# Kernel optimization log

Measured on AMD Instinct MI355X. Metric: run time of the kernel, lower is better.

Reference implementation:

```python
import jax, jax.numpy as jnp
import numpy as np
from jax import lax

B, S, NX, NSFC, H, NY = 8192, 64, 4, 5, 32, 1


def _lstm(x, h0, c0, w_ih, w_hh, b_ih, b_hh):
    """batch_first LSTM, PyTorch gate order (i, f, g, o).
    x: [B,S,I]; h0,c0: [B,H]; w_ih: [4H,I]; w_hh: [4H,H]. Returns [B,S,H]."""
    # Precompute the input projection for all timesteps (big GEMM, once).
    xg = jnp.einsum('bsi,gi->bsg', x, w_ih) + b_ih + b_hh  # [B,S,4H]

    def step(carry, xg_t):
        h, c = carry
        gates = xg_t + h @ w_hh.T  # [B,4H]
        i, f, g, o = jnp.split(gates, 4, axis=-1)
        i = jax.nn.sigmoid(i)
        f = jax.nn.sigmoid(f)
        g = jnp.tanh(g)
        o = jax.nn.sigmoid(o)
        c = f * c + i * g
        h = o * jnp.tanh(c)
        return (h, c), h

    (_, _), hs = lax.scan(step, (h0, c0), jnp.swapaxes(xg, 0, 1))  # hs: [S,B,H]
    return jnp.swapaxes(hs, 0, 1)


def setup_inputs() -> dict:
    key = jax.random.key(0)
    ks = jax.random.split(key, 16)
    s = 1.0 / np.sqrt(H)

    def u(k, shape):
        return jax.random.uniform(k, shape, jnp.float32, -s, s)

    return {
        'inputs_main': jax.random.normal(ks[0], (B, S, NX), jnp.float32),
        'inputs_sfc': jax.random.normal(ks[1], (B, NSFC), jnp.float32),
        'w_sfc1': u(ks[2], (H, NSFC)), 'b_sfc1': u(ks[3], (H,)),
        'w_sfc2': u(ks[4], (H, NSFC)), 'b_sfc2': u(ks[5], (H,)),
        'w_ih1': u(ks[6], (4 * H, NX)), 'w_hh1': u(ks[7], (4 * H, H)),
        'b_ih1': u(ks[8], (4 * H,)), 'b_hh1': u(ks[9], (4 * H,)),
        'w_ih2': u(ks[10], (4 * H, H)), 'w_hh2': u(ks[11], (4 * H, H)),
        'b_ih2': u(ks[12], (4 * H,)), 'b_hh2': u(ks[13], (4 * H,)),
        'w_out': u(ks[14], (NY, H)), 'b_out': u(ks[15], (NY,)),
    }


def reference(inputs_main, inputs_sfc,
              w_sfc1, b_sfc1, w_sfc2, b_sfc2,
              w_ih1, w_hh1, b_ih1, b_hh1,
              w_ih2, w_hh2, b_ih2, b_hh2,
              w_out, b_out):
    # Surface MLPs -> initial (h0, c0) of rnn1
    h0 = jnp.tanh(inputs_sfc @ w_sfc1.T + b_sfc1)  # [B,H]
    c0 = jnp.tanh(inputs_sfc @ w_sfc2.T + b_sfc2)  # [B,H]

    # rnn1 runs on time-reversed input; its output is flipped back
    x = jnp.flip(inputs_main, axis=1)
    out = _lstm(x, h0, c0, w_ih1, w_hh1, b_ih1, b_hh1)
    out = jnp.flip(out, axis=1)

    # rnn2 with zero initial state (PyTorch default)
    z = jnp.zeros((out.shape[0], H), out.dtype)
    out2 = _lstm(out, z, z, w_ih2, w_hh2, b_ih2, b_hh2)

    # Output MLP (concat=False -> last layer output only)
    return out2 @ w_out.T + b_out  # [B,S,NY]
```

## Files before the change

### kernel.cpp

```cpp
#include <hip/hip_runtime.h>

typedef __attribute__((ext_vector_type(4))) float f32x4;
typedef __attribute__((ext_vector_type(8))) short bf16x8;

#define LOG2E 1.44269504088896340736f

__device__ __forceinline__ float bcf(unsigned u){ union{unsigned u;float f;}v; v.u=u; return v.f; }
__device__ __forceinline__ unsigned pkbf(float a, float b){
    unsigned w; asm("v_cvt_pk_bf16_f32 %0, %1, %2" : "=v"(w) : "v"(a), "v"(b)); return w;
}
__device__ __forceinline__ float ex2(float x){ return __builtin_amdgcn_exp2f(x); }
__device__ __forceinline__ float rcp_(float x){ return __builtin_amdgcn_rcpf(x); }

#define MFMA(a,b,c) __builtin_amdgcn_mfma_f32_16x16x32_bf16(a,b,c,0,0,0)

union FragU { unsigned w[4]; bf16x8 v; };

__device__ __forceinline__ void split8(const float* v, bf16x8 &fh, bf16x8 &fl){
    FragU H, L;
#pragma unroll
    for (int i=0;i<4;i++){
        unsigned w = pkbf(v[2*i], v[2*i+1]);
        H.w[i] = w;
        float ra = v[2*i]   - bcf(w<<16);
        float rb = v[2*i+1] - bcf(w & 0xffff0000u);
        L.w[i] = pkbf(ra, rb);
    }
    fh = H.v; fl = L.v;
}

__device__ __forceinline__ void build_bx(const float4& x, int hi, FragU& B){
    unsigned w0 = pkbf(x.x, x.y), w1 = pkbf(x.z, x.w);
    float r0 = x.x - bcf(w0<<16), r1 = x.y - bcf(w0 & 0xffff0000u);
    float r2 = x.z - bcf(w1<<16), r3 = x.w - bcf(w1 & 0xffff0000u);
    unsigned l0 = pkbf(r0,r1), l1 = pkbf(r2,r3);
    const bool h01 = (hi < 2);
    B.w[0] = h01 ? w0 : 0u;
    B.w[1] = h01 ? w1 : 0u;
    B.w[2] = (hi==0) ? l0 : (hi==1 ? 0x3f803f80u : 0u);
    B.w[3] = (hi==0) ? l1 : 0u;
}

__device__ __forceinline__ void write_h(unsigned (*hb)[16][20], int b15, int hi, int wv_,
                                        const float* hv){
    unsigned h0 = pkbf(hv[0], hv[1]);
    unsigned h1 = pkbf(hv[2], hv[3]);
    float r0 = hv[0]-bcf(h0<<16), r1 = hv[1]-bcf(h0 & 0xffff0000u);
    float r2 = hv[2]-bcf(h1<<16), r3 = hv[3]-bcf(h1 & 0xffff0000u);
    unsigned l0 = pkbf(r0,r1), l1 = pkbf(r2,r3);
    const int wi = 8*wv_ + 2*hi;
    *(uint2*)&hb[0][b15][wi] = make_uint2(h0,h1);
    *(uint2*)&hb[1][b15][wi] = make_uint2(l0,l1);
}

__global__ __launch_bounds__(128) void lstm2_mfma2(
    const float* __restrict__ xin,
    const float* __restrict__ sfc,
    const float* __restrict__ w_sfc1, const float* __restrict__ b_sfc1,
    const float* __restrict__ w_sfc2, const float* __restrict__ b_sfc2,
    const float* __restrict__ w_ih1, const float* __restrict__ w_hh1,
    const float* __restrict__ b_ih1, const float* __restrict__ b_hh1,
    const float* __restrict__ w_ih2, const float* __restrict__ w_hh2,
    const float* __restrict__ b_ih2, const float* __restrict__ b_hh2,
    const float* __restrict__ w_out, const float* __restrict__ b_out,
    float* __restrict__ outp)
{
    __shared__ __align__(16) unsigned out1q[64][16][16];
    __shared__ __align__(16) unsigned hbuf[2][2][16][20];
    __shared__ float ybuf[2][64][16];

    const int tid  = threadIdx.x;
    const int wv   = tid >> 6;
    const int lane = tid & 63;
    const int b15  = lane & 15;
    const int hi   = (lane >> 4) & 3;
    const int B0   = blockIdx.x * 16;

    bf16x8 Whh_h[4], Whh_l[4], WxA[4];
    bf16x8 W2h_h[4], W2h_l[4], W2x_h[4], W2x_l[4];
    float bia[4][4], woutr[4];
#pragma unroll
    for (int c=0;c<4;c++){
        const int gr = 32*c + 16*wv + b15;
        const float sc = (c==2) ? (2.0f*LOG2E) : (-LOG2E);
        float wvv[8];
        {
            float4 wa = *(const float4*)(w_hh1 + gr*32 + 8*hi);
            float4 wb = *(const float4*)(w_hh1 + gr*32 + 8*hi + 4);
            wvv[0]=wa.x*sc; wvv[1]=wa.y*sc; wvv[2]=wa.z*sc; wvv[3]=wa.w*sc;
            wvv[4]=wb.x*sc; wvv[5]=wb.y*sc; wvv[6]=wb.z*sc; wvv[7]=wb.w*sc;
        }
        split8(wvv, Whh_h[c], Whh_l[c]);
        {
            float4 wi = *(const float4*)(w_ih1 + gr*4);
            float wh0=wi.x*sc, wh1=wi.y*sc, wh2=wi.z*sc, wh3=wi.w*sc;
            unsigned xw0 = pkbf(wh0,wh1), xw1 = pkbf(wh2,wh3);
            float wl0 = wh0-bcf(xw0<<16), wl1 = wh1-bcf(xw0 & 0xffff0000u);
            float wl2 = wh2-bcf(xw1<<16), wl3 = wh3-bcf(xw1 & 0xffff0000u);
            unsigned lw0 = pkbf(wl0,wl1), lw1 = pkbf(wl2,wl3);
            float bias = (b_ih1[gr] + b_hh1[gr])*sc;
            unsigned bh = pkbf(bias, 0.0f);
            float blo = bias - bcf(bh<<16);
            unsigned bword = pkbf(bias, blo);
            FragU A;
            if (hi==0){ A.w[0]=xw0; A.w[1]=xw1; A.w[2]=xw0; A.w[3]=xw1; }
            else if (hi==1){ A.w[0]=lw0; A.w[1]=lw1; A.w[2]=bword; A.w[3]=0u; }
            else { A.w[0]=0u; A.w[1]=0u; A.w[2]=0u; A.w[3]=0u; }
            WxA[c] = A.v;
        }
        {
            float4 wa = *(const float4*)(w_hh2 + gr*32 + 8*hi);
            float4 wb = *(const float4*)(w_hh2 + gr*32 + 8*hi + 4);
            wvv[0]=wa.x*sc; wvv[1]=wa.y*sc; wvv[2]=wa.z*sc; wvv[3]=wa.w*sc;
            wvv[4]=wb.x*sc; wvv[5]=wb.y*sc; wvv[6]=wb.z*sc; wvv[7]=wb.w*sc;
        }
        split8(wvv, W2h_h[c], W2h_l[c]);
        {
            const float scx = sc * (1.0f/32767.0f);
            float4 wa = *(const float4*)(w_ih2 + gr*32 + 8*hi);
            float4 wb = *(const float4*)(w_ih2 + gr*32 + 8*hi + 4);
            wvv[0]=wa.x*scx; wvv[1]=wa.y*scx; wvv[2]=wa.z*scx; wvv[3]=wa.w*scx;
            wvv[4]=wb.x*scx; wvv[5]=wb.y*scx; wvv[6]=wb.z*scx; wvv[7]=wb.w*scx;
        }
        split8(wvv, W2x_h[c], W2x_l[c]);
    }
#pragma unroll
    for (int p=0;p<4;p++){
        const int j = 16*wv + 4*hi + p;
        bia[0][p] = (b_ih2[j]    + b_hh2[j])    * (-LOG2E);
        bia[1][p] = (b_ih2[32+j] + b_hh2[32+j]) * (-LOG2E);
        bia[2][p] = (b_ih2[64+j] + b_hh2[64+j]) * (2.0f*LOG2E);
        bia[3][p] = (b_ih2[96+j] + b_hh2[96+j]) * (-LOG2E);
        woutr[p]  = w_out[j];
    }

    float cs[4], hv[4];
    {
        const float* sp = sfc + (B0 + b15)*5;
        const float s0=sp[0], s1=sp[1], s2=sp[2], s3=sp[3], s4=sp[4];
#pragma unroll
        for (int p=0;p<4;p++){
            const int j = 16*wv + 4*hi + p;
            float a1 = b_sfc1[j] + s0*w_sfc1[j*5+0] + s1*w_sfc1[j*5+1]
                     + s2*w_sfc1[j*5+2] + s3*w_sfc1[j*5+3] + s4*w_sfc1[j*5+4];
            float a2 = b_sfc2[j] + s0*w_sfc2[j*5+0] + s1*w_sfc2[j*5+1]
                     + s2*w_sfc2[j*5+2] + s3*w_sfc2[j*5+3] + s4*w_sfc2[j*5+4];
            hv[p] = 1.0f - 2.0f*rcp_(ex2((2.0f*LOG2E)*a1)+1.0f);
            cs[p] = (2.0f*LOG2E)*(1.0f - 2.0f*rcp_(ex2((2.0f*LOG2E)*a2)+1.0f));
        }
    }
    write_h(hbuf[0], b15, hi, wv, hv);
    __syncthreads();

    int par = 0;
    FragU Bx;
    {
        float4 x0 = *(const float4*)(xin + ((B0 + b15)*64 + 63)*4);
        build_bx(x0, hi, Bx);
    }
#pragma unroll 1
    for (int t=63; t>=0; --t){
        bf16x8 Hh = *(const bf16x8*)&hbuf[par][0][b15][4*hi];
        bf16x8 Hl = *(const bf16x8*)&hbuf[par][1][b15][4*hi];
        f32x4 acc[4];
#pragma unroll
        for (int c=0;c<4;c++){
            f32x4 a = {0.f,0.f,0.f,0.f};
            a = MFMA(WxA[c],   Bx.v, a);
            a = MFMA(Whh_h[c], Hh,   a);
            a = MFMA(Whh_h[c], Hl,   a);
            a = MFMA(Whh_l[c], Hh,   a);
            acc[c] = a;
        }
        if (t){
            float4 xn = *(const float4*)(xin + ((B0 + b15)*64 + (t-1))*4);
            build_bx(xn, hi, Bx);
        }
        int q[4];
#pragma unroll
        for (int p=0;p<4;p++){
            float iv = acc[0][p], fv = acc[1][p], gv = acc[2][p], ov = acc[3][p];
            float si = rcp_(1.0f+ex2(iv));
            float sf = rcp_(1.0f+ex2(fv));
            float so = rcp_(1.0f+ex2(ov));
            float tg = 1.0f - 2.0f*rcp_(ex2(gv)+1.0f);
            cs[p] = fmaf(sf, cs[p], ((2.0f*LOG2E)*si)*tg);
            float tc = 1.0f - 2.0f*rcp_(ex2(cs[p])+1.0f);
            hv[p] = so*tc;
            q[p] = __float2int_rn(hv[p]*32767.0f);
        }
        unsigned q01 = ((unsigned)q[0] & 0xffffu) | ((unsigned)q[1] << 16);
        unsigned q23 = ((unsigned)q[2] & 0xffffu) | ((unsigned)q[3] << 16);
        *(uint2*)&out1q[t][b15][8*wv + 2*hi] = make_uint2(q01, q23);
        write_h(hbuf[par^1], b15, hi, wv, hv);
        __syncthreads();
        par ^= 1;
    }

    {
        const int wi = 8*wv + 2*hi;
        *(uint2*)&hbuf[par][0][b15][wi] = make_uint2(0u,0u);
        *(uint2*)&hbuf[par][1][b15][wi] = make_uint2(0u,0u);
        cs[0]=0.f; cs[1]=0.f; cs[2]=0.f; cs[3]=0.f;
    }
    FragU Xh, Xl;
    {
        const uint4 xw = *(const uint4*)&out1q[0][b15][4*hi];
        float xv[8];
        xv[0]=(float)(short)(xw.x & 0xffffu); xv[1]=(float)((int)xw.x >> 16);
        xv[2]=(float)(short)(xw.y & 0xffffu); xv[3]=(float)((int)xw.y >> 16);
        xv[4]=(float)(short)(xw.z & 0xffffu); xv[5]=(float)((int)xw.z >> 16);
        xv[6]=(float)(short)(xw.w & 0xffffu); xv[7]=(float)((int)xw.w >> 16);
        split8(xv, Xh.v, Xl.v);
    }
    __syncthreads();

#pragma unroll 1
    for (int t=0; t<64; ++t){
        bf16x8 Hh = *(const bf16x8*)&hbuf[par][0][b15][4*hi];
        bf16x8 Hl = *(const bf16x8*)&hbuf[par][1][b15][4*hi];
        f32x4 acc[4];
#pragma unroll
        for (int c=0;c<4;c++){
            f32x4 a = {0.f,0.f,0.f,0.f};
            a = MFMA(W2x_h[c], Xh.v, a);
            a = MFMA(W2x_h[c], Xl.v, a);
            a = MFMA(W2x_l[c], Xh.v, a);
            a = MFMA(W2h_h[c], Hh,   a);
            a = MFMA(W2h_h[c], Hl,   a);
            a = MFMA(W2h_l[c], Hh,   a);
            acc[c] = a;
        }
        const int tn = (t < 63) ? t+1 : 63;
        const uint4 xw = *(const uint4*)&out1q[tn][b15][4*hi];

        float y = 0.0f;
#pragma unroll
        for (int p=0;p<4;p++){
            float iv = acc[0][p] + bia[0][p];
            float fv = acc[1][p] + bia[1][p];
            float gv = acc[2][p] + bia[2][p];
            float ov = acc[3][p] + bia[3][p];
            float si = rcp_(1.0f+ex2(iv));
            float sf = rcp_(1.0f+ex2(fv));
            float so = rcp_(1.0f+ex2(ov));
            float tg = 1.0f - 2.0f*rcp_(ex2(gv)+1.0f);
            cs[p] = fmaf(sf, cs[p], ((2.0f*LOG2E)*si)*tg);
            float tc = 1.0f - 2.0f*rcp_(ex2(cs[p])+1.0f);
            hv[p] = so*tc;
            y = fmaf(hv[p], woutr[p], y);
        }
        y += __shfl_xor(y, 16, 64);
        y += __shfl_xor(y, 32, 64);
        if (hi == 0) ybuf[wv][t][b15] = y;
        write_h(hbuf[par^1], b15, hi, wv, hv);
        {
            float xv[8];
            xv[0]=(float)(short)(xw.x & 0xffffu); xv[1]=(float)((int)xw.x >> 16);
            xv[2]=(float)(short)(xw.y & 0xffffu); xv[3]=(float)((int)xw.y >> 16);
            xv[4]=(float)(short)(xw.z & 0xffffu); xv[5]=(float)((int)xw.z >> 16);
            xv[6]=(float)(short)(xw.w & 0xffffu); xv[7]=(float)((int)xw.w >> 16);
            split8(xv, Xh.v, Xl.v);
        }
        __syncthreads();
        par ^= 1;
    }

    const float bo = b_out[0];
    const int bb = tid >> 3;
    const int t0 = (tid & 7) * 8;
#pragma unroll
    for (int hlf=0; hlf<2; ++hlf){
        float4 v;
        v.x = ybuf[0][t0+4*hlf+0][bb] + ybuf[1][t0+4*hlf+0][bb] + bo;
        v.y = ybuf[0][t0+4*hlf+1][bb] + ybuf[1][t0+4*hlf+1][bb] + bo;
        v.z = ybuf[0][t0+4*hlf+2][bb] + ybuf[1][t0+4*hlf+2][bb] + bo;
        v.w = ybuf[0][t0+4*hlf+3][bb] + ybuf[1][t0+4*hlf+3][bb] + bo;
        *(float4*)(outp + (B0 + bb)*64 + t0 + 4*hlf) = v;
    }
}

extern "C" void kernel_launch(void* const* d_in, const int* in_sizes, int n_in,
                              void* d_out, int out_size, void* d_ws, size_t ws_size,
                              hipStream_t stream) {
    const float* xin    = (const float*)d_in[0];
    const float* sfc    = (const float*)d_in[1];
    const float* w_sfc1 = (const float*)d_in[2];
    const float* b_sfc1 = (const float*)d_in[3];
    const float* w_sfc2 = (const float*)d_in[4];
    const float* b_sfc2 = (const float*)d_in[5];
    const float* w_ih1  = (const float*)d_in[6];
    const float* w_hh1  = (const float*)d_in[7];
    const float* b_ih1  = (const float*)d_in[8];
    const float* b_hh1  = (const float*)d_in[9];
    const float* w_ih2  = (const float*)d_in[10];
    const float* w_hh2  = (const float*)d_in[11];
    const float* b_ih2  = (const float*)d_in[12];
    const float* b_hh2  = (const float*)d_in[13];
    const float* w_out  = (const float*)d_in[14];
    const float* b_out  = (const float*)d_in[15];
    float* out = (float*)d_out;

    dim3 grid(8192 / 16);
    dim3 block(128);
    hipLaunchKernelGGL(lstm2_mfma2, grid, block, 0, stream,
                       xin, sfc, w_sfc1, b_sfc1, w_sfc2, b_sfc2,
                       w_ih1, w_hh1, b_ih1, b_hh1,
                       w_ih2, w_hh2, b_ih2, b_hh2,
                       w_out, b_out, out);
}
```

Baseline: 175.1 us.

## Split gate work across four waves and spill layer-1 output to workspace

Adds a 256-thread kernel where each of four waves computes two gate-column MFMA tiles instead of four, with the gate layout rearranged so each lane holds all four gates of one hidden unit. The quantized layer-1 hidden sequence now goes to a global workspace instead of a 64 KB shared buffer, which cuts LDS use per block so more blocks can be resident. Layer-2 weights are loaded after layer 1 to lower register pressure. The old kernel is kept as a fallback when the workspace is too small. The costs are global-memory round trips for the layer-1 sequence and scalar 16-bit LDS stores for the hidden state.

After: 182.6 us. +4.3%, slower.

```diff
diff --git a/kernel.cpp b/kernel.cpp
--- a/kernel.cpp
+++ b/kernel.cpp
@@ -41,21 +41,265 @@
     B.w[3] = (hi==0) ? l1 : 0u;
 }
 
-__device__ __forceinline__ void write_h(unsigned (*hb)[16][20], int b15, int hi, int wv_,
-                                        const float* hv){
-    unsigned h0 = pkbf(hv[0], hv[1]);
-    unsigned h1 = pkbf(hv[2], hv[3]);
-    float r0 = hv[0]-bcf(h0<<16), r1 = hv[1]-bcf(h0 & 0xffff0000u);
-    float r2 = hv[2]-bcf(h1<<16), r3 = hv[3]-bcf(h1 & 0xffff0000u);
+__device__ __forceinline__ void put_h(unsigned* Hh, unsigned* Hl, int col, int j, float h){
+    unsigned w  = pkbf(h, 0.0f);
+    float  rr   = h - bcf(w << 16);
+    unsigned lw = pkbf(rr, 0.0f);
+    ((unsigned short*)Hh)[col*40 + j] = (unsigned short)w;
+    ((unsigned short*)Hl)[col*40 + j] = (unsigned short)lw;
+}
+
+__global__ __launch_bounds__(256) void lstm2_q(
+    const float* __restrict__ xin,
+    const float* __restrict__ sfc,
+    const float* __restrict__ w_sfc1, const float* __restrict__ b_sfc1,
+    const float* __restrict__ w_sfc2, const float* __restrict__ b_sfc2,
+    const float* __restrict__ w_ih1, const float* __restrict__ w_hh1,
+    const float* __restrict__ b_ih1, const float* __restrict__ b_hh1,
+    const float* __restrict__ w_ih2, const float* __restrict__ w_hh2,
+    const float* __restrict__ b_ih2, const float* __restrict__ b_hh2,
+    const float* __restrict__ w_out, const float* __restrict__ b_out,
+    float* __restrict__ outp,
+    unsigned* __restrict__ ws)
+{
+    __shared__ __align__(16) unsigned hbuf[2][2][16][20];
+    __shared__ float ybuf[4][64][16];
+
+    const int tid  = threadIdx.x;
+    const int wq   = tid >> 6;
+    const int lane = tid & 63;
+    const int col  = lane & 15;
+    const int hi   = lane >> 4;
+    const int B0   = blockIdx.x * 16;
+    unsigned* wsb  = ws + blockIdx.x * 16384;
+
+    const int jl = col >> 2, g = col & 3;
+    const float sc = (g == 2) ? (2.0f*LOG2E) : (-LOG2E);
+    const int j0 = 8*wq + hi;
+    const int j1 = 8*wq + 4 + hi;
+
+    bf16x8 Whh_h[2], Whh_l[2], WxA[2];
+#pragma unroll
+    for (int c=0;c<2;c++){
+        const int grow = g*32 + 8*wq + 4*c + jl;
+        float wvv[8];
+        float4 wa = *(const float4*)(w_hh1 + grow*32 + 8*hi);
+        float4 wb = *(const float4*)(w_hh1 + grow*32 + 8*hi + 4);
+        wvv[0]=wa.x*sc; wvv[1]=wa.y*sc; wvv[2]=wa.z*sc; wvv[3]=wa.w*sc;
+        wvv[4]=wb.x*sc; wvv[5]=wb.y*sc; wvv[6]=wb.z*sc; wvv[7]=wb.w*sc;
+        split8(wvv, Whh_h[c], Whh_l[c]);
+        float4 wi = *(const float4*)(w_ih1 + grow*4);
+        float wh0=wi.x*sc, wh1=wi.y*sc, wh2=wi.z*sc, wh3=wi.w*sc;
+        unsigned xw0 = pkbf(wh0,wh1), xw1 = pkbf(wh2,wh3);
+        float wl0 = wh0-bcf(xw0<<16), wl1 = wh1-bcf(xw0 & 0xffff0000u);
+        float wl2 = wh2-bcf(xw1<<16), wl3 = wh3-bcf(xw1 & 0xffff0000u);
+        unsigned lw0 = pkbf(wl0,wl1), lw1 = pkbf(wl2,wl3);
+        float bias = (b_ih1[grow] + b_hh1[grow])*sc;
+        unsigned bh = pkbf(bias, 0.0f);
+        float blo = bias - bcf(bh<<16);
+        unsigned bword = pkbf(bias, blo);
+        FragU A;
+        if (hi==0){ A.w[0]=xw0; A.w[1]=xw1; A.w[2]=xw0; A.w[3]=xw1; }
+        else if (hi==1){ A.w[0]=lw0; A.w[1]=lw1; A.w[2]=bword; A.w[3]=0u; }
+        else { A.w[0]=0u; A.w[1]=0u; A.w[2]=0u; A.w[3]=0u; }
+        WxA[c] = A.v;
+    }
+
+    float cs[2], hv[2];
+    {
+        const float* sp = sfc + (B0 + col)*5;
+        const float s0=sp[0], s1=sp[1], s2=sp[2], s3=sp[3], s4=sp[4];
+#pragma unroll
+        for (int c=0;c<2;c++){
+            const int j = 8*wq + 4*c + hi;
+            float a1 = b_sfc1[j] + s0*w_sfc1[j*5+0] + s1*w_sfc1[j*5+1]
+                     + s2*w_sfc1[j*5+2] + s3*w_sfc1[j*5+3] + s4*w_sfc1[j*5+4];
+            float a2 = b_sfc2[j] + s0*w_sfc2[j*5+0] + s1*w_sfc2[j*5+1]
+                     + s2*w_sfc2[j*5+2] + s3*w_sfc2[j*5+3] + s4*w_sfc2[j*5+4];
+            hv[c] = 1.0f - 2.0f*rcp_(ex2((2.0f*LOG2E)*a1)+1.0f);
+            cs[c] = (2.0f*LOG2E)*(1.0f - 2.0f*rcp_(ex2((2.0f*LOG2E)*a2)+1.0f));
+        }
+    }
+    put_h(&hbuf[0][0][0][0], &hbuf[0][1][0][0], col, j0, hv[0]);
+    put_h(&hbuf[0][0][0][0], &hbuf[0][1][0][0], col, j1, hv[1]);
+    __syncthreads();
+
+    int par = 0;
+    FragU Bx;
+    {
+        float4 x0 = *(const float4*)(xin + ((B0 + col)*64 + 63)*4);
+        build_bx(x0, hi, Bx);
+    }
+#pragma unroll 1
+    for (int t=63; t>=0; --t){
+        bf16x8 Hh = *(const bf16x8*)&hbuf[par][0][col][4*hi];
+        bf16x8 Hl = *(const bf16x8*)&hbuf[par][1][col][4*hi];
+        f32x4 acc[2];
+#pragma unroll
+        for (int c=0;c<2;c++){
+            f32x4 a = {0.f,0.f,0.f,0.f};
+            a = MFMA(WxA[c],   Bx.v, a);
+            a = MFMA(Whh_h[c], Hh,   a);
+            a = MFMA(Whh_h[c], Hl,   a);
+            a = MFMA(Whh_l[c], Hh,   a);
+            acc[c] = a;
+        }
+        if (t){
+            float4 xn = *(const float4*)(xin + ((B0 + col)*64 + (t-1))*4);
+            build_bx(xn, hi, Bx);
+        }
+        int q[2];
+#pragma unroll
+        for (int c=0;c<2;c++){
+            float iv = acc[c][0], fv = acc[c][1], gv = acc[c][2], ov = acc[c][3];
+            float si = rcp_(1.0f+ex2(iv));
+            float sf = rcp_(1.0f+ex2(fv));
+            float so = rcp_(1.0f+ex2(ov));
+            float tg = 1.0f - 2.0f*rcp_(ex2(gv)+1.0f);
+            cs[c] = fmaf(sf, cs[c], ((2.0f*LOG2E)*si)*tg);
+            float tc = 1.0f - 2.0f*rcp_(ex2(cs[c])+1.0f);
+            hv[c] = so*tc;
+            q[c] = __float2int_rn(hv[c]*32767.0f);
+        }
+        put_h(&hbuf[par^1][0][0][0], &hbuf[par^1][1][0][0], col, j0, hv[0]);
+        put_h(&hbuf[par^1][0][0][0], &hbuf[par^1][1][0][0], col, j1, hv[1]);
+        {
+            int e0 = __shfl_xor(q[0], 16, 64);
+            int e1 = __shfl_xor(q[1], 16, 64);
+            unsigned val = (hi & 1)
+                ? (((unsigned)e1 & 0xffffu) | ((unsigned)q[1] << 16))
+                : (((unsigned)q[0] & 0xffffu) | ((unsigned)e0 << 16));
+            const int word = 4*wq + 2*(hi & 1) + (hi >> 1);
+            wsb[(t*16 + col)*16 + word] = val;
+        }
+        __syncthreads();
+        par ^= 1;
+    }
+
+    bf16x8 W2h_h[2], W2h_l[2], W2x_h[2], W2x_l[2];
+#pragma unroll
+    for (int c=0;c<2;c++){
+        const int grow = g*32 + 8*wq + 4*c + jl;
+        float wvv[8];
+        {
+            float4 wa = *(const float4*)(w_hh2 + grow*32 + 8*hi);
+            float4 wb = *(const float4*)(w_hh2 + grow*32 + 8*hi + 4);
+            wvv[0]=wa.x*sc; wvv[1]=wa.y*sc; wvv[2]=wa.z*sc; wvv[3]=wa.w*sc;
+            wvv[4]=wb.x*sc; wvv[5]=wb.y*sc; wvv[6]=wb.z*sc; wvv[7]=wb.w*sc;
+        }
+        split8(wvv, W2h_h[c], W2h_l[c]);
+        {
+            const float scx = sc * (1.0f/32767.0f);
+            float4 wa = *(const float4*)(w_ih2 + grow*32 + 8*hi);
+            float4 wb = *(const float4*)(w_ih2 + grow*32 + 8*hi + 4);
+            wvv[0]=wa.x*scx; wvv[1]=wa.y*scx; wvv[2]=wa.z*scx; wvv[3]=wa.w*scx;
+            wvv[4]=wb.x*scx; wvv[5]=wb.y*scx; wvv[6]=wb.z*scx; wvv[7]=wb.w*scx;
+        }
+        split8(wvv, W2x_h[c], W2x_l[c]);
+    }
+    float bia[2][4], woutr[2];
+#pragma unroll
+    for (int c=0;c<2;c++){
+        const int j = 8*wq + 4*c + hi;
+#pragma unroll
+        for (int p=0;p<4;p++){
+            const float s = (p==2) ? (2.0f*LOG2E) : (-LOG2E);
+            bia[c][p] = (b_ih2[p*32+j] + b_hh2[p*32+j]) * s;
+        }
+        woutr[c] = w_out[j];
+        cs[c] = 0.0f;
+    }
+    put_h(&hbuf[par][0][0][0], &hbuf[par][1][0][0], col, j0, 0.0f);
+    put_h(&hbuf[par][0][0][0], &hbuf[par][1][0][0], col, j1, 0.0f);
+    FragU Xh, Xl;
+    {
+        const uint4 xw = *(const uint4*)&wsb[(0*16 + col)*16 + 4*hi];
+        float xv[8];
+        xv[0]=(float)(short)(xw.x & 0xffffu); xv[1]=(float)((int)xw.x >> 16);
+        xv[2]=(float)(short)(xw.y & 0xffffu); xv[3]=(float)((int)xw.y >> 16);
+        xv[4]=(float)(short)(xw.z & 0xffffu); xv[5]=(float)((int)xw.z >> 16);
+        xv[6]=(float)(short)(xw.w & 0xffffu); xv[7]=(float)((int)xw.w >> 16);
+        split8(xv, Xh.v, Xl.v);
+    }
+    __syncthreads();
+
+#pragma unroll 1
+    for (int t=0; t<64; ++t){
+        bf16x8 Hh = *(const bf16x8*)&hbuf[par][0][col][4*hi];
+        bf16x8 Hl = *(const bf16x8*)&hbuf[par][1][col][4*hi];
+        f32x4 acc[2];
+#pragma unroll
+        for (int c=0;c<2;c++){
+            f32x4 a = {0.f,0.f,0.f,0.f};
+            a = MFMA(W2x_h[c], Xh.v, a);
+            a = MFMA(W2x_h[c], Xl.v, a);
+            a = MFMA(W2x_l[c], Xh.v, a);
+            a = MFMA(W2h_h[c], Hh,   a);
+            a = MFMA(W2h_h[c], Hl,   a);
+            a = MFMA(W2h_l[c], Hh,   a);
+            acc[c] = a;
+        }
+        const int tn = (t < 63) ? t+1 : 63;
+        const uint4 xw = *(const uint4*)&wsb[(tn*16 + col)*16 + 4*hi];
+
+        float y = 0.0f;
+#pragma unroll
+        for (int c=0;c<2;c++){
+            float iv = acc[c][0] + bia[c][0];
+            float fv = acc[c][1] + bia[c][1];
+            float gv = acc[c][2] + bia[c][2];
+            float ov = acc[c][3] + bia[c][3];
+            float si = rcp_(1.0f+ex2(iv));
+            float sf = rcp_(1.0f+ex2(fv));
+            float so = rcp_(1.0f+ex2(ov));
+            float tg = 1.0f - 2.0f*rcp_(ex2(gv)+1.0f);
+            cs[c] = fmaf(sf, cs[c], ((2.0f*LOG2E)*si)*tg);
+            float tc = 1.0f - 2.0f*rcp_(ex2(cs[c])+1.0f);
+            hv[c] = so*tc;
+            y = fmaf(hv[c], woutr[c], y);
+        }
+        y += __shfl_xor(y, 16, 64);
+        y += __shfl_xor(y, 32, 64);
+        if (hi == 0) ybuf[wq][t][col] = y;
+        put_h(&hbuf[par^1][0][0][0], &hbuf[par^1][1][0][0], col, j0, hv[0]);
+        put_h(&hbuf[par^1][0][0][0], &hbuf[par^1][1][0][0], col, j1, hv[1]);
+        {
+            float xv[8];
+            xv[0]=(float)(short)(xw.x & 0xffffu); xv[1]=(float)((int)xw.x >> 16);
+            xv[2]=(float)(short)(xw.y & 0xffffu); xv[3]=(float)((int)xw.y >> 16);
+            xv[4]=(float)(short)(xw.z & 0xffffu); xv[5]=(float)((int)xw.z >> 16);
+            xv[6]=(float)(short)(xw.w & 0xffffu); xv[7]=(float)((int)xw.w >> 16);
+            split8(xv, Xh.v, Xl.v);
+        }
+        __syncthreads();
+        par ^= 1;
+    }
+
+    const float bo = b_out[0];
+    const int bb = tid >> 4;
+    const int t0 = (tid & 15) * 4;
+    float4 v;
+    v.x = ybuf[0][t0+0][bb]+ybuf[1][t0+0][bb]+ybuf[2][t0+0][bb]+ybuf[3][t0+0][bb]+bo;
+    v.y = ybuf[0][t0+1][bb]+ybuf[1][t0+1][bb]+ybuf[2][t0+1][bb]+ybuf[3][t0+1][bb]+bo;
+    v.z = ybuf[0][t0+2][bb]+ybuf[1][t0+2][bb]+ybuf[2][t0+2][bb]+ybuf[3][t0+2][bb]+bo;
+    v.w = ybuf[0][t0+3][bb]+ybuf[1][t0+3][bb]+ybuf[2][t0+3][bb]+ybuf[3][t0+3][bb]+bo;
+    *(float4*)(outp + (B0 + bb)*64 + t0) = v;
+}
+
+__device__ __forceinline__ void write_h_pair(unsigned (*hb)[16][20], int b15, int hi, int wv_,
+                                             const float* hvv){
+    unsigned h0 = pkbf(hvv[0], hvv[1]);
+    unsigned h1 = pkbf(hvv[2], hvv[3]);
+    float r0 = hvv[0]-bcf(h0<<16), r1 = hvv[1]-bcf(h0 & 0xffff0000u);
+    float r2 = hvv[2]-bcf(h1<<16), r3 = hvv[3]-bcf(h1 & 0xffff0000u);
     unsigned l0 = pkbf(r0,r1), l1 = pkbf(r2,r3);
     const int wi = 8*wv_ + 2*hi;
     *(uint2*)&hb[0][b15][wi] = make_uint2(h0,h1);
     *(uint2*)&hb[1][b15][wi] = make_uint2(l0,l1);
 }
 
-__global__ __launch_bounds__(128) void lstm2_mfma2(
-    const float* __restrict__ xin,
-    const float* __restrict__ sfc,
+__global__ __launch_bounds__(128) void lstm2_fb(
+    const float* __restrict__ xin, const float* __restrict__ sfc,
     const float* __restrict__ w_sfc1, const float* __restrict__ b_sfc1,
     const float* __restrict__ w_sfc2, const float* __restrict__ b_sfc2,
     const float* __restrict__ w_ih1, const float* __restrict__ w_hh1,
@@ -68,14 +312,12 @@
     __shared__ __align__(16) unsigned out1q[64][16][16];
     __shared__ __align__(16) unsigned hbuf[2][2][16][20];
     __shared__ float ybuf[2][64][16];
-
     const int tid  = threadIdx.x;
     const int wv   = tid >> 6;
     const int lane = tid & 63;
     const int b15  = lane & 15;
     const int hi   = (lane >> 4) & 3;
     const int B0   = blockIdx.x * 16;
-
     bf16x8 Whh_h[4], Whh_l[4], WxA[4];
     bf16x8 W2h_h[4], W2h_l[4], W2x_h[4], W2x_l[4];
     float bia[4][4], woutr[4];
@@ -133,8 +375,7 @@
         bia[3][p] = (b_ih2[96+j] + b_hh2[96+j]) * (-LOG2E);
         woutr[p]  = w_out[j];
     }
-
-    float cs[4], hv[4];
+    float cs[4], hvv[4];
     {
         const float* sp = sfc + (B0 + b15)*5;
         const float s0=sp[0], s1=sp[1], s2=sp[2], s3=sp[3], s4=sp[4];
@@ -145,13 +386,12 @@
                      + s2*w_sfc1[j*5+2] + s3*w_sfc1[j*5+3] + s4*w_sfc1[j*5+4];
             float a2 = b_sfc2[j] + s0*w_sfc2[j*5+0] + s1*w_sfc2[j*5+1]
                      + s2*w_sfc2[j*5+2] + s3*w_sfc2[j*5+3] + s4*w_sfc2[j*5+4];
-            hv[p] = 1.0f - 2.0f*rcp_(ex2((2.0f*LOG2E)*a1)+1.0f);
+            hvv[p] = 1.0f - 2.0f*rcp_(ex2((2.0f*LOG2E)*a1)+1.0f);
             cs[p] = (2.0f*LOG2E)*(1.0f - 2.0f*rcp_(ex2((2.0f*LOG2E)*a2)+1.0f));
         }
     }
-    write_h(hbuf[0], b15, hi, wv, hv);
+    write_h_pair(hbuf[0], b15, hi, wv, hvv);
     __syncthreads();
-
     int par = 0;
     FragU Bx;
     {
@@ -186,17 +426,16 @@
             float tg = 1.0f - 2.0f*rcp_(ex2(gv)+1.0f);
             cs[p] = fmaf(sf, cs[p], ((2.0f*LOG2E)*si)*tg);
             float tc = 1.0f - 2.0f*rcp_(ex2(cs[p])+1.0f);
-            hv[p] = so*tc;
-            q[p] = __float2int_rn(hv[p]*32767.0f);
+            hvv[p] = so*tc;
+            q[p] = __float2int_rn(hvv[p]*32767.0f);
         }
         unsigned q01 = ((unsigned)q[0] & 0xffffu) | ((unsigned)q[1] << 16);
         unsigned q23 = ((unsigned)q[2] & 0xffffu) | ((unsigned)q[3] << 16);
         *(uint2*)&out1q[t][b15][8*wv + 2*hi] = make_uint2(q01, q23);
-        write_h(hbuf[par^1], b15, hi, wv, hv);
+        write_h_pair(hbuf[par^1], b15, hi, wv, hvv);
         __syncthreads();
         par ^= 1;
     }
-
     {
         const int wi = 8*wv + 2*hi;
         *(uint2*)&hbuf[par][0][b15][wi] = make_uint2(0u,0u);
@@ -214,7 +453,6 @@
         split8(xv, Xh.v, Xl.v);
     }
     __syncthreads();
-
 #pragma unroll 1
     for (int t=0; t<64; ++t){
         bf16x8 Hh = *(const bf16x8*)&hbuf[par][0][b15][4*hi];
@@ -233,7 +471,6 @@
         }
         const int tn = (t < 63) ? t+1 : 63;
         const uint4 xw = *(const uint4*)&out1q[tn][b15][4*hi];
-
         float y = 0.0f;
 #pragma unroll
         for (int p=0;p<4;p++){
@@ -247,13 +484,13 @@
             float tg = 1.0f - 2.0f*rcp_(ex2(gv)+1.0f);
             cs[p] = fmaf(sf, cs[p], ((2.0f*LOG2E)*si)*tg);
             float tc = 1.0f - 2.0f*rcp_(ex2(cs[p])+1.0f);
-            hv[p] = so*tc;
-            y = fmaf(hv[p], woutr[p], y);
+            hvv[p] = so*tc;
+            y = fmaf(hvv[p], woutr[p], y);
         }
         y += __shfl_xor(y, 16, 64);
         y += __shfl_xor(y, 32, 64);
         if (hi == 0) ybuf[wv][t][b15] = y;
-        write_h(hbuf[par^1], b15, hi, wv, hv);
+        write_h_pair(hbuf[par^1], b15, hi, wv, hvv);
         {
             float xv[8];
             xv[0]=(float)(short)(xw.x & 0xffffu); xv[1]=(float)((int)xw.x >> 16);
@@ -265,7 +502,6 @@
         __syncthreads();
         par ^= 1;
     }
-
     const float bo = b_out[0];
     const int bb = tid >> 3;
     const int t0 = (tid & 7) * 8;
@@ -301,11 +537,18 @@
     const float* b_out  = (const float*)d_in[15];
     float* out = (float*)d_out;
 
-    dim3 grid(8192 / 16);
-    dim3 block(128);
-    hipLaunchKernelGGL(lstm2_mfma2, grid, block, 0, stream,
-                       xin, sfc, w_sfc1, b_sfc1, w_sfc2, b_sfc2,
-                       w_ih1, w_hh1, b_ih1, b_hh1,
-                       w_ih2, w_hh2, b_ih2, b_hh2,
-                       w_out, b_out, out);
-}
+    const size_t need = 512ull * 65536ull;
+    if (ws_size >= need) {
+        hipLaunchKernelGGL(lstm2_q, dim3(512), dim3(256), 0, stream,
+                           xin, sfc, w_sfc1, b_sfc1, w_sfc2, b_sfc2,
+                           w_ih1, w_hh1, b_ih1, b_hh1,
+                           w_ih2, w_hh2, b_ih2, b_hh2,
+                           w_out, b_out, out, (unsigned*)d_ws);
+    } else {
+        hipLaunchKernelGGL(lstm2_fb, dim3(512), dim3(128), 0, stream,
+                           xin, sfc, w_sfc1, b_sfc1, w_sfc2, b_sfc2,
+                           w_ih1, w_hh1, b_ih1, b_hh1,
+                           w_ih2, w_hh2, b_ih2, b_hh2,
+                           w_out, b_out, out);
+    }
+}
```

## Split LSTM gates across 8 waves per block and spill layer-1 output to workspace

Applied to the files above, without the earlier changes.

Each block now runs 8 waves instead of 2, and each wave computes one gate row-slice with a single MFMA tile per step, so one lane holds one hidden unit's four gates instead of four units. The per-step MFMA chain is split into two independent accumulators. The quantized layer-1 output moves from shared memory to a global workspace, which frees LDS for more resident waves. The idea is to shorten the serial per-timestep critical path and raise occupancy, at the cost of global-memory traffic and barriers across more waves.

New measurement: 198.8 us. 1.14x slower.

```diff
diff --git a/kernel.cpp b/kernel.cpp
--- a/kernel.cpp
+++ b/kernel.cpp
@@ -4,6 +4,7 @@
 typedef __attribute__((ext_vector_type(8))) short bf16x8;
 
 #define LOG2E 1.44269504088896340736f
+#define BAR_LGKM() asm volatile("s_waitcnt lgkmcnt(0)\n\ts_barrier" ::: "memory")
 
 __device__ __forceinline__ float bcf(unsigned u){ union{unsigned u;float f;}v; v.u=u; return v.f; }
 __device__ __forceinline__ unsigned pkbf(float a, float b){
@@ -41,19 +42,24 @@
     B.w[3] = (hi==0) ? l1 : 0u;
 }
 
-__device__ __forceinline__ void write_h(unsigned (*hb)[16][20], int b15, int hi, int wv_,
-                                        const float* hv){
-    unsigned h0 = pkbf(hv[0], hv[1]);
-    unsigned h1 = pkbf(hv[2], hv[3]);
-    float r0 = hv[0]-bcf(h0<<16), r1 = hv[1]-bcf(h0 & 0xffff0000u);
-    float r2 = hv[2]-bcf(h1<<16), r3 = hv[3]-bcf(h1 & 0xffff0000u);
-    unsigned l0 = pkbf(r0,r1), l1 = pkbf(r2,r3);
-    const int wi = 8*wv_ + 2*hi;
-    *(uint2*)&hb[0][b15][wi] = make_uint2(h0,h1);
-    *(uint2*)&hb[1][b15][wi] = make_uint2(l0,l1);
-}
-
-__global__ __launch_bounds__(128) void lstm2_mfma2(
+__device__ __forceinline__ void dec_q(const uint4& xw, FragU& Xh, FragU& Xl){
+    float xv[8];
+    xv[0]=(float)(short)(xw.x & 0xffffu); xv[1]=(float)((int)xw.x >> 16);
+    xv[2]=(float)(short)(xw.y & 0xffffu); xv[3]=(float)((int)xw.y >> 16);
+    xv[4]=(float)(short)(xw.z & 0xffffu); xv[5]=(float)((int)xw.z >> 16);
+    xv[6]=(float)(short)(xw.w & 0xffffu); xv[7]=(float)((int)xw.w >> 16);
+    split8(xv, Xh.v, Xl.v);
+}
+
+__device__ __forceinline__ void put_h1(unsigned (*hb)[16][20], int col, int j, float h){
+    unsigned wpk = pkbf(h, 0.0f);
+    float rr = h - bcf(wpk<<16);
+    unsigned lw = pkbf(rr, 0.0f);
+    ((unsigned short*)hb[0])[col*40 + j] = (unsigned short)wpk;
+    ((unsigned short*)hb[1])[col*40 + j] = (unsigned short)lw;
+}
+
+__global__ __launch_bounds__(512, 4) void lstm2_o(
     const float* __restrict__ xin,
     const float* __restrict__ sfc,
     const float* __restrict__ w_sfc1, const float* __restrict__ b_sfc1,
@@ -63,221 +69,175 @@
     const float* __restrict__ w_ih2, const float* __restrict__ w_hh2,
     const float* __restrict__ b_ih2, const float* __restrict__ b_hh2,
     const float* __restrict__ w_out, const float* __restrict__ b_out,
-    float* __restrict__ outp)
+    float* __restrict__ outp,
+    unsigned* __restrict__ ws)
 {
-    __shared__ __align__(16) unsigned out1q[64][16][16];
     __shared__ __align__(16) unsigned hbuf[2][2][16][20];
-    __shared__ float ybuf[2][64][16];
+    __shared__ float ybuf[8][64][16];
 
     const int tid  = threadIdx.x;
-    const int wv   = tid >> 6;
+    const int w    = tid >> 6;
     const int lane = tid & 63;
-    const int b15  = lane & 15;
-    const int hi   = (lane >> 4) & 3;
+    const int col  = lane & 15;
+    const int hi   = lane >> 4;
     const int B0   = blockIdx.x * 16;
-
-    bf16x8 Whh_h[4], Whh_l[4], WxA[4];
-    bf16x8 W2h_h[4], W2h_l[4], W2x_h[4], W2x_l[4];
-    float bia[4][4], woutr[4];
-#pragma unroll
-    for (int c=0;c<4;c++){
-        const int gr = 32*c + 16*wv + b15;
-        const float sc = (c==2) ? (2.0f*LOG2E) : (-LOG2E);
+    unsigned* wsb  = ws + blockIdx.x * 16384;
+
+    const int jl = col >> 2, g = col & 3;
+    const float sc = (g == 2) ? (2.0f*LOG2E) : (-LOG2E);
+    const int j    = 4*w + hi;
+    const int grow = g*32 + 4*w + jl;
+
+    bf16x8 Whh_h, Whh_l, WxA;
+    {
+        float wvv[8];
+        float4 wa = *(const float4*)(w_hh1 + grow*32 + 8*hi);
+        float4 wb = *(const float4*)(w_hh1 + grow*32 + 8*hi + 4);
+        wvv[0]=wa.x*sc; wvv[1]=wa.y*sc; wvv[2]=wa.z*sc; wvv[3]=wa.w*sc;
+        wvv[4]=wb.x*sc; wvv[5]=wb.y*sc; wvv[6]=wb.z*sc; wvv[7]=wb.w*sc;
+        split8(wvv, Whh_h, Whh_l);
+        float4 wi = *(const float4*)(w_ih1 + grow*4);
+        float wh0=wi.x*sc, wh1=wi.y*sc, wh2=wi.z*sc, wh3=wi.w*sc;
+        unsigned xw0 = pkbf(wh0,wh1), xw1 = pkbf(wh2,wh3);
+        float wl0 = wh0-bcf(xw0<<16), wl1 = wh1-bcf(xw0 & 0xffff0000u);
+        float wl2 = wh2-bcf(xw1<<16), wl3 = wh3-bcf(xw1 & 0xffff0000u);
+        unsigned lw0 = pkbf(wl0,wl1), lw1 = pkbf(wl2,wl3);
+        float bias = (b_ih1[grow] + b_hh1[grow])*sc;
+        unsigned bh = pkbf(bias, 0.0f);
+        float blo = bias - bcf(bh<<16);
+        unsigned bword = pkbf(bias, blo);
+        FragU A;
+        if (hi==0){ A.w[0]=xw0; A.w[1]=xw1; A.w[2]=xw0; A.w[3]=xw1; }
+        else if (hi==1){ A.w[0]=lw0; A.w[1]=lw1; A.w[2]=bword; A.w[3]=0u; }
+        else { A.w[0]=0u; A.w[1]=0u; A.w[2]=0u; A.w[3]=0u; }
+        WxA = A.v;
+    }
+    bf16x8 W2h_h, W2h_l, W2x_h, W2x_l;
+    {
         float wvv[8];
         {
-            float4 wa = *(const float4*)(w_hh1 + gr*32 + 8*hi);
-            float4 wb = *(const float4*)(w_hh1 + gr*32 + 8*hi + 4);
+            float4 wa = *(const float4*)(w_hh2 + grow*32 + 8*hi);
+            float4 wb = *(const float4*)(w_hh2 + grow*32 + 8*hi + 4);
             wvv[0]=wa.x*sc; wvv[1]=wa.y*sc; wvv[2]=wa.z*sc; wvv[3]=wa.w*sc;
             wvv[4]=wb.x*sc; wvv[5]=wb.y*sc; wvv[6]=wb.z*sc; wvv[7]=wb.w*sc;
         }
-        split8(wvv, Whh_h[c], Whh_l[c]);
-        {
-            float4 wi = *(const float4*)(w_ih1 + gr*4);
-            float wh0=wi.x*sc, wh1=wi.y*sc, wh2=wi.z*sc, wh3=wi.w*sc;
-            unsigned xw0 = pkbf(wh0,wh1), xw1 = pkbf(wh2,wh3);
-            float wl0 = wh0-bcf(xw0<<16), wl1 = wh1-bcf(xw0 & 0xffff0000u);
-            float wl2 = wh2-bcf(xw1<<16), wl3 = wh3-bcf(xw1 & 0xffff0000u);
-            unsigned lw0 = pkbf(wl0,wl1), lw1 = pkbf(wl2,wl3);
-            float bias = (b_ih1[gr] + b_hh1[gr])*sc;
-            unsigned bh = pkbf(bias, 0.0f);
-            float blo = bias - bcf(bh<<16);
-            unsigned bword = pkbf(bias, blo);
-            FragU A;
-            if (hi==0){ A.w[0]=xw0; A.w[1]=xw1; A.w[2]=xw0; A.w[3]=xw1; }
-            else if (hi==1){ A.w[0]=lw0; A.w[1]=lw1; A.w[2]=bword; A.w[3]=0u; }
-            else { A.w[0]=0u; A.w[1]=0u; A.w[2]=0u; A.w[3]=0u; }
-            WxA[c] = A.v;
-        }
-        {
-            float4 wa = *(const float4*)(w_hh2 + gr*32 + 8*hi);
-            float4 wb = *(const float4*)(w_hh2 + gr*32 + 8*hi + 4);
-            wvv[0]=wa.x*sc; wvv[1]=wa.y*sc; wvv[2]=wa.z*sc; wvv[3]=wa.w*sc;
-            wvv[4]=wb.x*sc; wvv[5]=wb.y*sc; wvv[6]=wb.z*sc; wvv[7]=wb.w*sc;
-        }
-        split8(wvv, W2h_h[c], W2h_l[c]);
+        split8(wvv, W2h_h, W2h_l);
         {
             const float scx = sc * (1.0f/32767.0f);
-            float4 wa = *(const float4*)(w_ih2 + gr*32 + 8*hi);
-            float4 wb = *(const float4*)(w_ih2 + gr*32 + 8*hi + 4);
+            float4 wa = *(const float4*)(w_ih2 + grow*32 + 8*hi);
+            float4 wb = *(const float4*)(w_ih2 + grow*32 + 8*hi + 4);
             wvv[0]=wa.x*scx; wvv[1]=wa.y*scx; wvv[2]=wa.z*scx; wvv[3]=wa.w*scx;
             wvv[4]=wb.x*scx; wvv[5]=wb.y*scx; wvv[6]=wb.z*scx; wvv[7]=wb.w*scx;
         }
-        split8(wvv, W2x_h[c], W2x_l[c]);
-    }
+        split8(wvv, W2x_h, W2x_l);
+    }
+    float bia[4], woutj;
 #pragma unroll
     for (int p=0;p<4;p++){
-        const int j = 16*wv + 4*hi + p;
-        bia[0][p] = (b_ih2[j]    + b_hh2[j])    * (-LOG2E);
-        bia[1][p] = (b_ih2[32+j] + b_hh2[32+j]) * (-LOG2E);
-        bia[2][p] = (b_ih2[64+j] + b_hh2[64+j]) * (2.0f*LOG2E);
-        bia[3][p] = (b_ih2[96+j] + b_hh2[96+j]) * (-LOG2E);
-        woutr[p]  = w_out[j];
-    }
-
-    float cs[4], hv[4];
-    {
-        const float* sp = sfc + (B0 + b15)*5;
+        const float s = (p==2) ? (2.0f*LOG2E) : (-LOG2E);
+        bia[p] = (b_ih2[p*32+j] + b_hh2[p*32+j]) * s;
+    }
+    woutj = w_out[j];
+
+    float cs, hv;
+    {
+        const float* sp = sfc + (B0 + col)*5;
         const float s0=sp[0], s1=sp[1], s2=sp[2], s3=sp[3], s4=sp[4];
-#pragma unroll
-        for (int p=0;p<4;p++){
-            const int j = 16*wv + 4*hi + p;
-            float a1 = b_sfc1[j] + s0*w_sfc1[j*5+0] + s1*w_sfc1[j*5+1]
-                     + s2*w_sfc1[j*5+2] + s3*w_sfc1[j*5+3] + s4*w_sfc1[j*5+4];
-            float a2 = b_sfc2[j] + s0*w_sfc2[j*5+0] + s1*w_sfc2[j*5+1]
-                     + s2*w_sfc2[j*5+2] + s3*w_sfc2[j*5+3] + s4*w_sfc2[j*5+4];
-            hv[p] = 1.0f - 2.0f*rcp_(ex2((2.0f*LOG2E)*a1)+1.0f);
-            cs[p] = (2.0f*LOG2E)*(1.0f - 2.0f*rcp_(ex2((2.0f*LOG2E)*a2)+1.0f));
-        }
-    }
-    write_h(hbuf[0], b15, hi, wv, hv);
+        float a1 = b_sfc1[j] + s0*w_sfc1[j*5+0] + s1*w_sfc1[j*5+1]
+                 + s2*w_sfc1[j*5+2] + s3*w_sfc1[j*5+3] + s4*w_sfc1[j*5+4];
+        float a2 = b_sfc2[j] + s0*w_sfc2[j*5+0] + s1*w_sfc2[j*5+1]
+                 + s2*w_sfc2[j*5+2] + s3*w_sfc2[j*5+3] + s4*w_sfc2[j*5+4];
+        hv = 1.0f - 2.0f*rcp_(ex2((2.0f*LOG2E)*a1)+1.0f);
+        cs = (2.0f*LOG2E)*(1.0f - 2.0f*rcp_(ex2((2.0f*LOG2E)*a2)+1.0f));
+    }
+    put_h1(hbuf[0], col, j, hv);
     __syncthreads();
 
     int par = 0;
     FragU Bx;
     {
-        float4 x0 = *(const float4*)(xin + ((B0 + b15)*64 + 63)*4);
+        float4 x0 = *(const float4*)(xin + ((B0 + col)*64 + 63)*4);
         build_bx(x0, hi, Bx);
     }
 #pragma unroll 1
     for (int t=63; t>=0; --t){
-        bf16x8 Hh = *(const bf16x8*)&hbuf[par][0][b15][4*hi];
-        bf16x8 Hl = *(const bf16x8*)&hbuf[par][1][b15][4*hi];
-        f32x4 acc[4];
-#pragma unroll
-        for (int c=0;c<4;c++){
-            f32x4 a = {0.f,0.f,0.f,0.f};
-            a = MFMA(WxA[c],   Bx.v, a);
-            a = MFMA(Whh_h[c], Hh,   a);
-            a = MFMA(Whh_h[c], Hl,   a);
-            a = MFMA(Whh_l[c], Hh,   a);
-            acc[c] = a;
-        }
+        bf16x8 Hh = *(const bf16x8*)&hbuf[par][0][col][4*hi];
+        bf16x8 Hl = *(const bf16x8*)&hbuf[par][1][col][4*hi];
+        f32x4 a = {0.f,0.f,0.f,0.f}, b2 = {0.f,0.f,0.f,0.f};
+        a  = MFMA(WxA,   Bx.v, a);
+        b2 = MFMA(Whh_h, Hl,   b2);
+        a  = MFMA(Whh_h, Hh,   a);
+        b2 = MFMA(Whh_l, Hh,   b2);
         if (t){
-            float4 xn = *(const float4*)(xin + ((B0 + b15)*64 + (t-1))*4);
+            float4 xn = *(const float4*)(xin + ((B0 + col)*64 + (t-1))*4);
             build_bx(xn, hi, Bx);
         }
-        int q[4];
-#pragma unroll
-        for (int p=0;p<4;p++){
-            float iv = acc[0][p], fv = acc[1][p], gv = acc[2][p], ov = acc[3][p];
-            float si = rcp_(1.0f+ex2(iv));
-            float sf = rcp_(1.0f+ex2(fv));
-            float so = rcp_(1.0f+ex2(ov));
-            float tg = 1.0f - 2.0f*rcp_(ex2(gv)+1.0f);
-            cs[p] = fmaf(sf, cs[p], ((2.0f*LOG2E)*si)*tg);
-            float tc = 1.0f - 2.0f*rcp_(ex2(cs[p])+1.0f);
-            hv[p] = so*tc;
-            q[p] = __float2int_rn(hv[p]*32767.0f);
-        }
-        unsigned q01 = ((unsigned)q[0] & 0xffffu) | ((unsigned)q[1] << 16);
-        unsigned q23 = ((unsigned)q[2] & 0xffffu) | ((unsigned)q[3] << 16);
-        *(uint2*)&out1q[t][b15][8*wv + 2*hi] = make_uint2(q01, q23);
-        write_h(hbuf[par^1], b15, hi, wv, hv);
-        __syncthreads();
+        f32x4 acc = a + b2;
+        float si = rcp_(1.0f+ex2(acc[0]));
+        float sf = rcp_(1.0f+ex2(acc[1]));
+        float tg = 1.0f - 2.0f*rcp_(ex2(acc[2])+1.0f);
+        float so = rcp_(1.0f+ex2(acc[3]));
+        cs = fmaf(sf, cs, ((2.0f*LOG2E)*si)*tg);
+        float tc = 1.0f - 2.0f*rcp_(ex2(cs)+1.0f);
+        hv = so*tc;
+        put_h1(hbuf[par^1], col, j, hv);
+        int q = __float2int_rn(hv*32767.0f);
+        int e = __shfl_xor(q, 16, 64);
+        if (!(hi & 1)){
+            unsigned val = ((unsigned)q & 0xffffu) | ((unsigned)e << 16);
+            wsb[(t*16 + col)*16 + 2*w + (hi>>1)] = val;
+        }
+        BAR_LGKM();
         par ^= 1;
     }
 
-    {
-        const int wi = 8*wv + 2*hi;
-        *(uint2*)&hbuf[par][0][b15][wi] = make_uint2(0u,0u);
-        *(uint2*)&hbuf[par][1][b15][wi] = make_uint2(0u,0u);
-        cs[0]=0.f; cs[1]=0.f; cs[2]=0.f; cs[3]=0.f;
-    }
+    cs = 0.0f;
+    put_h1(hbuf[par], col, j, 0.0f);
+    __syncthreads();
     FragU Xh, Xl;
     {
-        const uint4 xw = *(const uint4*)&out1q[0][b15][4*hi];
-        float xv[8];
-        xv[0]=(float)(short)(xw.x & 0xffffu); xv[1]=(float)((int)xw.x >> 16);
-        xv[2]=(float)(short)(xw.y & 0xffffu); xv[3]=(float)((int)xw.y >> 16);
-        xv[4]=(float)(short)(xw.z & 0xffffu); xv[5]=(float)((int)xw.z >> 16);
-        xv[6]=(float)(short)(xw.w & 0xffffu); xv[7]=(float)((int)xw.w >> 16);
-        split8(xv, Xh.v, Xl.v);
-    }
-    __syncthreads();
+        const uint4 xw = *(const uint4*)&wsb[(0*16 + col)*16 + 4*hi];
+        dec_q(xw, Xh, Xl);
+    }
 
 #pragma unroll 1
     for (int t=0; t<64; ++t){
-        bf16x8 Hh = *(const bf16x8*)&hbuf[par][0][b15][4*hi];
-        bf16x8 Hl = *(const bf16x8*)&hbuf[par][1][b15][4*hi];
-        f32x4 acc[4];
-#pragma unroll
-        for (int c=0;c<4;c++){
-            f32x4 a = {0.f,0.f,0.f,0.f};
-            a = MFMA(W2x_h[c], Xh.v, a);
-            a = MFMA(W2x_h[c], Xl.v, a);
-            a = MFMA(W2x_l[c], Xh.v, a);
-            a = MFMA(W2h_h[c], Hh,   a);
-            a = MFMA(W2h_h[c], Hl,   a);
-            a = MFMA(W2h_l[c], Hh,   a);
-            acc[c] = a;
-        }
+        bf16x8 Hh = *(const bf16x8*)&hbuf[par][0][col][4*hi];
+        bf16x8 Hl = *(const bf16x8*)&hbuf[par][1][col][4*hi];
+        f32x4 a = {0.f,0.f,0.f,0.f}, b2 = {0.f,0.f,0.f,0.f};
+        a  = MFMA(W2x_h, Xh.v, a);
+        b2 = MFMA(W2h_h, Hh,   b2);
+        a  = MFMA(W2x_h, Xl.v, a);
+        b2 = MFMA(W2h_h, Hl,   b2);
+        a  = MFMA(W2x_l, Xh.v, a);
+        b2 = MFMA(W2h_l, Hh,   b2);
         const int tn = (t < 63) ? t+1 : 63;
-        const uint4 xw = *(const uint4*)&out1q[tn][b15][4*hi];
-
-        float y = 0.0f;
-#pragma unroll
-        for (int p=0;p<4;p++){
-            float iv = acc[0][p] + bia[0][p];
-            float fv = acc[1][p] + bia[1][p];
-            float gv = acc[2][p] + bia[2][p];
-            float ov = acc[3][p] + bia[3][p];
-            float si = rcp_(1.0f+ex2(iv));
-            float sf = rcp_(1.0f+ex2(fv));
-            float so = rcp_(1.0f+ex2(ov));
-            float tg = 1.0f - 2.0f*rcp_(ex2(gv)+1.0f);
-            cs[p] = fmaf(sf, cs[p], ((2.0f*LOG2E)*si)*tg);
-            float tc = 1.0f - 2.0f*rcp_(ex2(cs[p])+1.0f);
-            hv[p] = so*tc;
-            y = fmaf(hv[p], woutr[p], y);
-        }
+        const uint4 xw = *(const uint4*)&wsb[(tn*16 + col)*16 + 4*hi];
+        f32x4 acc = a + b2;
+        float si = rcp_(1.0f+ex2(acc[0]+bia[0]));
+        float sf = rcp_(1.0f+ex2(acc[1]+bia[1]));
+        float tg = 1.0f - 2.0f*rcp_(ex2(acc[2]+bia[2])+1.0f);
+        float so = rcp_(1.0f+ex2(acc[3]+bia[3]));
+        cs = fmaf(sf, cs, ((2.0f*LOG2E)*si)*tg);
+        float tc = 1.0f - 2.0f*rcp_(ex2(cs)+1.0f);
+        hv = so*tc;
+        float y = hv * woutj;
         y += __shfl_xor(y, 16, 64);
         y += __shfl_xor(y, 32, 64);
-        if (hi == 0) ybuf[wv][t][b15] = y;
-        write_h(hbuf[par^1], b15, hi, wv, hv);
-        {
-            float xv[8];
-            xv[0]=(float)(short)(xw.x & 0xffffu); xv[1]=(float)((int)xw.x >> 16);
-            xv[2]=(float)(short)(xw.y & 0xffffu); xv[3]=(float)((int)xw.y >> 16);
-            xv[4]=(float)(short)(xw.z & 0xffffu); xv[5]=(float)((int)xw.z >> 16);
-            xv[6]=(float)(short)(xw.w & 0xffffu); xv[7]=(float)((int)xw.w >> 16);
-            split8(xv, Xh.v, Xl.v);
-        }
-        __syncthreads();
+        if (hi == 0) ybuf[w][t][col] = y;
+        put_h1(hbuf[par^1], col, j, hv);
+        dec_q(xw, Xh, Xl);
+        BAR_LGKM();
         par ^= 1;
     }
 
     const float bo = b_out[0];
-    const int bb = tid >> 3;
-    const int t0 = (tid & 7) * 8;
+    const int bb = tid >> 5;
+    const int t0 = (tid & 31) * 2;
+    float s0 = bo, s1 = bo;
 #pragma unroll
-    for (int hlf=0; hlf<2; ++hlf){
-        float4 v;
-        v.x = ybuf[0][t0+4*hlf+0][bb] + ybuf[1][t0+4*hlf+0][bb] + bo;
-        v.y = ybuf[0][t0+4*hlf+1][bb] + ybuf[1][t0+4*hlf+1][bb] + bo;
-        v.z = ybuf[0][t0+4*hlf+2][bb] + ybuf[1][t0+4*hlf+2][bb] + bo;
-        v.w = ybuf[0][t0+4*hlf+3][bb] + ybuf[1][t0+4*hlf+3][bb] + bo;
-        *(float4*)(outp + (B0 + bb)*64 + t0 + 4*hlf) = v;
-    }
+    for (int u=0; u<8; ++u){ s0 += ybuf[u][t0][bb]; s1 += ybuf[u][t0+1][bb]; }
+    *(float2*)(outp + (B0 + bb)*64 + t0) = make_float2(s0, s1);
 }
 
 extern "C" void kernel_launch(void* const* d_in, const int* in_sizes, int n_in,
@@ -301,11 +261,9 @@
     const float* b_out  = (const float*)d_in[15];
     float* out = (float*)d_out;
 
-    dim3 grid(8192 / 16);
-    dim3 block(128);
-    hipLaunchKernelGGL(lstm2_mfma2, grid, block, 0, stream,
+    hipLaunchKernelGGL(lstm2_o, dim3(512), dim3(512), 0, stream,
                        xin, sfc, w_sfc1, b_sfc1, w_sfc2, b_sfc2,
                        w_ih1, w_hh1, b_ih1, b_hh1,
                        w_ih2, w_hh2, b_ih2, b_hh2,
-                       w_out, b_out, out);
-}
+                       w_out, b_out, out, (unsigned*)d_ws);
+}
```
